# Optimization experiments

Measured on AMD Instinct MI355X. Metric: run time of the kernel, lower is better.

## Reference

```python
import jax, jax.numpy as jnp
import numpy as np

N_NODES = 30000
N_EDGES = 150000
N_REL = 10
IN_DIM = 256
OUT_DIM = 256


def setup_inputs() -> dict:
    key = jax.random.key(0)
    ks = jax.random.split(key, 10)
    s = 1.0 / np.sqrt(IN_DIM)  # ~nn.Linear init scale
    return {
        "x": jax.random.normal(ks[0], (N_NODES, IN_DIM), jnp.float32),
        "W_self": jax.random.uniform(ks[1], (IN_DIM, OUT_DIM), jnp.float32, -s, s),
        "b_self": jax.random.uniform(ks[2], (OUT_DIM,), jnp.float32, -s, s),
        "W_fwd": jax.random.uniform(ks[3], (N_REL, IN_DIM, OUT_DIM), jnp.float32, -s, s),
        "b_fwd": jax.random.uniform(ks[4], (N_REL, OUT_DIM), jnp.float32, -s, s),
        "W_rev": jax.random.uniform(ks[5], (N_REL, IN_DIM, OUT_DIM), jnp.float32, -s, s),
        "b_rev": jax.random.uniform(ks[6], (N_REL, OUT_DIM), jnp.float32, -s, s),
        "dep_idx": jax.random.randint(ks[7], (N_EDGES,), 0, N_NODES, jnp.int32),
        "rel_idx": jax.random.randint(ks[8], (N_EDGES,), 0, N_REL, jnp.int32),
        "gov_idx": jax.random.randint(ks[9], (N_EDGES,), 0, N_NODES, jnp.int32),
    }


def reference(x, W_self, b_self, W_fwd, b_fwd, W_rev, b_rev, dep_idx, rel_idx, gov_idx):
    # self transform for every token: [N, out]
    out = x @ W_self + b_self
    # transform all nodes by every relation weight up-front: [R, N, out]
    H_fwd = jnp.einsum("ni,rio->rno", x, W_fwd) + b_fwd[:, None, :]
    H_rev = jnp.einsum("ni,rio->rno", x, W_rev) + b_rev[:, None, :]
    # per-edge gather: forward msg uses governor feature, reverse msg uses dependent
    msg_fwd = H_fwd[rel_idx, gov_idx]  # [E, out]
    msg_rev = H_rev[rel_idx, dep_idx]  # [E, out]
    # scatter-add: forward msg -> dependent, reverse msg -> governor
    out = out.at[dep_idx].add(msg_fwd)
    out = out.at[gov_idx].add(msg_rev)
    return out
```

## Files before the change

kernel.cpp:

```cpp
#include <hip/hip_runtime.h>

#define N_NODES 30000
#define N_EDGES 150000
#define N_REL 10
#define DIM 256

#define SORT_BLOCKS 120
#define SORT_CHUNK ((N_EDGES + SORT_BLOCKS - 1) / SORT_BLOCKS)

#define SCAN_CHUNK 256
#define SCAN_BLOCKS ((N_NODES + SCAN_CHUNK - 1) / SCAN_CHUNK)

#define PREP_XB 7500
#define PREP_WB 5376
#define PREP_ZB 235

typedef __attribute__((ext_vector_type(8))) short bf16x8;
typedef __attribute__((ext_vector_type(4))) float f32x4;

__device__ __forceinline__ unsigned short f2bf(float f) {
  union { float f; unsigned int u; } v; v.f = f;
  unsigned int u = v.u;
  unsigned int r = u + 0x7fffu + ((u >> 16) & 1u);
  return (unsigned short)(r >> 16);
}


__global__ void prep_kernel(const float* __restrict__ x,
                            const float* __restrict__ Wf,
                            const float* __restrict__ Wr,
                            const float* __restrict__ Ws,
                            unsigned short* __restrict__ xbf,
                            unsigned short* __restrict__ wt,
                            int* __restrict__ cnt) {
  int b = blockIdx.x;
  if (b < PREP_XB) {
    int idx = b * 256 + threadIdx.x;
    float4 v = reinterpret_cast<const float4*>(x)[idx];
    ushort4 o;
    o.x = f2bf(v.x); o.y = f2bf(v.y); o.z = f2bf(v.z); o.w = f2bf(v.w);
    reinterpret_cast<ushort4*>(xbf)[idx] = o;
  } else if (b < PREP_XB + PREP_WB) {
    int idx = (b - PREP_XB) * 256 + threadIdx.x;
    int bb = idx >> 16;
    int t = idx & 65535;
    int o = t >> 8, i = t & 255;
    const float* src = (bb < N_REL) ? (Wf + (size_t)bb * 65536)
                     : (bb < 2 * N_REL) ? (Wr + (size_t)(bb - N_REL) * 65536)
                     : Ws;
    wt[idx] = f2bf(src[i * 256 + o]);
  } else {
    int i = (b - PREP_XB - PREP_WB) * 256 + threadIdx.x;
    if (i < 2 * N_NODES) cnt[i] = 0;
  }
}

__global__ void hist_all_kernel(const int* __restrict__ rel,
                                const int* __restrict__ dep,
                                const int* __restrict__ gov,
                                int* __restrict__ block_counts,
                                int* __restrict__ cnt) {
  __shared__ int h[N_REL];
  if (threadIdx.x < N_REL) h[threadIdx.x] = 0;
  __syncthreads();
  int beg = blockIdx.x * SORT_CHUNK;
  int end = min(beg + SORT_CHUNK, N_EDGES);
  for (int e = beg + threadIdx.x; e < end; e += blockDim.x) {
    atomicAdd(&h[rel[e]], 1);
    atomicAdd(&cnt[dep[e]], 1);
    atomicAdd(&cnt[N_NODES + gov[e]], 1);
  }
  __syncthreads();
  if (threadIdx.x < N_REL)
    block_counts[blockIdx.x * N_REL + threadIdx.x] = h[threadIdx.x];
}

__global__ void scan_rel_kernel(const int* __restrict__ block_counts,
                                int* __restrict__ rel_start,
                                int* __restrict__ block_offset) {
  __shared__ int tot[N_REL];
  int r = threadIdx.x;
  if (r < N_REL) {
    int s = 0;
    for (int b = 0; b < SORT_BLOCKS; ++b) s += block_counts[b * N_REL + r];
    tot[r] = s;
  }
  __syncthreads();
  if (threadIdx.x == 0) {
    int s = 0;
    for (int i = 0; i < N_REL; ++i) { rel_start[i] = s; s += tot[i]; }
    rel_start[N_REL] = s;
  }
  __syncthreads();
  if (r < N_REL) {
    int run = rel_start[r];
    for (int b = 0; b < SORT_BLOCKS; ++b) {
      block_offset[b * N_REL + r] = run;
      run += block_counts[b * N_REL + r];
    }
  }
}

__global__ void scanA_kernel(const int* __restrict__ cnt,
                             int* __restrict__ tmp, int* __restrict__ sums) {
  __shared__ int s[SCAN_CHUNK];
  int d = blockIdx.y, b = blockIdx.x, t = threadIdx.x;
  int i = b * SCAN_CHUNK + t;
  int v = (i < N_NODES) ? cnt[d * N_NODES + i] : 0;
  s[t] = v;
  __syncthreads();
  for (int off = 1; off < SCAN_CHUNK; off <<= 1) {
    int add = (t >= off) ? s[t - off] : 0;
    __syncthreads();
    s[t] += add;
    __syncthreads();
  }
  if (i < N_NODES) tmp[d * N_NODES + i] = s[t] - v;
  if (t == SCAN_CHUNK - 1) sums[d * SCAN_BLOCKS + b] = s[t];
}

__global__ void scanB_kernel(const int* __restrict__ sums,
                             int* __restrict__ chunk_off, int* __restrict__ rp) {
  __shared__ int s[128];
  int d = blockIdx.x, t = threadIdx.x;
  int v = (t < SCAN_BLOCKS) ? sums[d * SCAN_BLOCKS + t] : 0;
  s[t] = v;
  __syncthreads();
  for (int off = 1; off < 128; off <<= 1) {
    int add = (t >= off) ? s[t - off] : 0;
    __syncthreads();
    s[t] += add;
    __syncthreads();
  }
  if (t < SCAN_BLOCKS) chunk_off[d * SCAN_BLOCKS + t] = s[t] - v;
  if (t == 127) rp[d * (N_NODES + 1) + N_NODES] = s[127];
}

__global__ void scanC_kernel(const int* __restrict__ tmp,
                             const int* __restrict__ chunk_off,
                             int* __restrict__ rp, int* __restrict__ cursor) {
  int d = blockIdx.y;
  int i = blockIdx.x * SCAN_CHUNK + threadIdx.x;
  if (i < N_NODES) {
    int v = tmp[d * N_NODES + i] + chunk_off[d * SCAN_BLOCKS + blockIdx.x];
    rp[d * (N_NODES + 1) + i] = v;
    cursor[d * N_NODES + i] = v;
  }
}

__global__ void scatter_all_kernel(const int* __restrict__ rel,
                                   const int* __restrict__ dep,
                                   const int* __restrict__ gov,
                                   const int* __restrict__ block_offset,
                                   int* __restrict__ cursor,
                                   int* __restrict__ perm,
                                   int* __restrict__ srcf,
                                   int* __restrict__ srcr,
                                   int* __restrict__ colf,
                                   int* __restrict__ colr) {
  __shared__ int cur[N_REL];
  if (threadIdx.x < N_REL)
    cur[threadIdx.x] = block_offset[blockIdx.x * N_REL + threadIdx.x];
  __syncthreads();
  int beg = blockIdx.x * SORT_CHUNK;
  int end = min(beg + SORT_CHUNK, N_EDGES);
  for (int e = beg + threadIdx.x; e < end; e += blockDim.x) {
    int dp = dep[e], gv = gov[e];
    int pos = atomicAdd(&cur[rel[e]], 1);
    perm[pos] = e;
    srcf[pos] = gv;
    srcr[pos] = dp;
    colf[atomicAdd(&cursor[dp], 1)] = pos;
    colr[atomicAdd(&cursor[N_NODES + gv], 1)] = pos;
  }
}


__global__ __launch_bounds__(256, 2)
void mega_gemm_kernel(const unsigned short* __restrict__ xbf,
                      const unsigned short* __restrict__ wt,
                      const float* __restrict__ b_self,
                      const float* __restrict__ b_fwd,
                      const float* __restrict__ b_rev,
                      const int* __restrict__ srcf,
                      const int* __restrict__ srcr,
                      const int* __restrict__ rel_start,
                      unsigned short* __restrict__ msg,
                      float* __restrict__ out) {
  const int bkt = blockIdx.y;
  const bool is_self = (bkt >= 2 * N_REL);
  const bool fwd = bkt < N_REL;
  const int r = is_self ? 0 : (fwd ? bkt : bkt - N_REL);

  int beg, cnt;
  const int* src_arr = fwd ? srcf : srcr;
  unsigned short* mdir = msg + (fwd ? 0 : (size_t)N_EDGES * DIM);
  if (is_self) {
    beg = (bkt - 2 * N_REL) * (N_NODES / 2);
    cnt = N_NODES / 2;
  } else {
    beg = rel_start[r];
    cnt = rel_start[r + 1] - beg;
  }
  const int ntiles = (cnt + 63) >> 6;
  const int GX = gridDim.x;

  const int tid = threadIdx.x;
  const int wave = tid >> 6, lane = tid & 63;
  const int lm = lane & 15, q = lane >> 4;
  const int nb = wave * 64;
  const int half = lane >> 5;

  __shared__ int s_src[2][64];
  __shared__ unsigned short sA[2][64 * DIM];

  bf16x8 wf[8][4];
  const unsigned short* wbase =
      wt + (size_t)(is_self ? 2 * N_REL : bkt) * DIM * DIM;
  #pragma unroll
  for (int kk = 0; kk < 8; ++kk)
    #pragma unroll
    for (int ni = 0; ni < 4; ++ni)
      wf[kk][ni] = *reinterpret_cast<const bf16x8*>(
          wbase + (size_t)(nb + ni * 16 + lm) * DIM + kk * 32 + q * 8);

  const float* bptr = is_self ? b_self : ((fwd ? b_fwd : b_rev) + r * DIM);
  float bias[4];
  #pragma unroll
  for (int ni = 0; ni < 4; ++ni) bias[ni] = bptr[nb + ni * 16 + lm];

  int swz[8];
  #pragma unroll
  for (int i = 0; i < 8; ++i)
    swz[i] = (((lane & 31) ^ ((i * 2 + half) & 7)) * 8);
  int rowoff[4];
  #pragma unroll
  for (int mi = 0; mi < 4; ++mi) rowoff[mi] = (mi * 16 + lm) * DIM;
  int ckoff[8];
  #pragma unroll
  for (int kk = 0; kk < 8; ++kk)
    ckoff[kk] = ((kk * 4 + q) ^ (lm & 7)) * 8;

  int t = blockIdx.x;
  if (t >= ntiles) return;

  auto load_idx = [&](int tt) -> int {
    int tile0_ = tt << 6;
    if (is_self) {
      int rr = beg + tile0_ + tid;
      return rr < beg + cnt ? rr : beg + cnt - 1;
    } else {
      int p_ = tile0_ + tid;
      p_ = p_ < cnt ? p_ : cnt - 1;
      return src_arr[beg + p_];
    }
  };

  auto issue_stage = [&](int p) {
    const int* sp = s_src[p];
    unsigned short* db = sA[p];
    #pragma unroll
    for (int i = 0; i < 8; ++i) {
      int ldsrow = wave * 16 + i * 2;
      int rr = sp[ldsrow + half];
      const unsigned short* g = xbf + (size_t)rr * DIM + swz[i];
      __builtin_amdgcn_global_load_lds(
          (const __attribute__((address_space(1))) void*)g,
          (__attribute__((address_space(3))) void*)(db + ldsrow * DIM),
          16, 0, 0);
    }
  };

  auto step = [&](int cur) {
    const int tile0 = t << 6;
    const int rows_valid = min(64, cnt - tile0);
    const bool have_next = (t + GX) < ntiles;
    const bool have_next2 = (t + 2 * GX) < ntiles;

    __syncthreads();
    if (have_next) issue_stage(cur ^ 1);
    if (tid < 64 && have_next2) s_src[cur][tid] = load_idx(t + 2 * GX);

    f32x4 acc[4][4];
    #pragma unroll
    for (int mi = 0; mi < 4; ++mi)
      #pragma unroll
      for (int ni = 0; ni < 4; ++ni)
        acc[mi][ni] = (f32x4){0.f, 0.f, 0.f, 0.f};

    const unsigned short* sAb = sA[cur];
    #pragma unroll
    for (int kk = 0; kk < 8; ++kk) {
      bf16x8 a[4];
      #pragma unroll
      for (int mi = 0; mi < 4; ++mi)
        a[mi] = *reinterpret_cast<const bf16x8*>(sAb + rowoff[mi] + ckoff[kk]);
      #pragma unroll
      for (int mi = 0; mi < 4; ++mi)
        #pragma unroll
        for (int ni = 0; ni < 4; ++ni)
          acc[mi][ni] = __builtin_amdgcn_mfma_f32_16x16x32_bf16(
              a[mi], wf[kk][ni], acc[mi][ni], 0, 0, 0);
    }

    if (is_self) {
      #pragma unroll
      for (int mi = 0; mi < 4; ++mi) {
        #pragma unroll
        for (int reg = 0; reg < 4; ++reg) {
          int row = mi * 16 + q * 4 + reg;
          if (row < rows_valid) {
            #pragma unroll
            for (int ni = 0; ni < 4; ++ni)
              out[(size_t)(beg + tile0 + row) * DIM + nb + ni * 16 + lm] =
                  acc[mi][ni][reg] + bias[ni];
          }
        }
      }
    } else {
      #pragma unroll
      for (int mi = 0; mi < 4; ++mi) {
        #pragma unroll
        for (int reg = 0; reg < 4; ++reg) {
          int row = mi * 16 + q * 4 + reg;
          if (row < rows_valid) {
            unsigned int p0 = ((unsigned int)f2bf(acc[mi][1][reg] + bias[1]) << 16) |
                              f2bf(acc[mi][0][reg] + bias[0]);
            unsigned int p1 = ((unsigned int)f2bf(acc[mi][3][reg] + bias[3]) << 16) |
                              f2bf(acc[mi][2][reg] + bias[2]);
            uint2 u; u.x = p0; u.y = p1;
            *reinterpret_cast<uint2*>(
                mdir + (size_t)(beg + tile0 + row) * DIM + nb + lm * 4) = u;
          }
        }
      }
    }
  };

  if (tid < 64) s_src[0][tid] = load_idx(t);
  __syncthreads();
  issue_stage(0);
  if (tid < 64 && t + GX < ntiles) s_src[1][tid] = load_idx(t + GX);

  while (true) {
    step(0);
    t += GX; if (t >= ntiles) break;
    step(1);
    t += GX; if (t >= ntiles) break;
  }
}


__global__ void reduce_both_kernel(const unsigned short* __restrict__ msg,
                                   const int* __restrict__ rp,
                                   const int* __restrict__ colf,
                                   const int* __restrict__ colr,
                                   float* __restrict__ out) {
  const int n = blockIdx.x, t = threadIdx.x;
  const int g = t >> 6, lane = t & 63;
  const int b0 = rp[n], e0 = rp[n + 1];
  const int b1 = rp[(N_NODES + 1) + n], e1 = rp[(N_NODES + 1) + n + 1];
  if (e0 <= b0 && e1 <= b1) return;

  float a0 = 0.f, a1 = 0.f, a2 = 0.f, a3 = 0.f;
  for (int j = b0 + g; j < e0; j += 4) {
    int row = colf[j];
    uint2 v = *reinterpret_cast<const uint2*>(msg + (size_t)row * DIM + lane * 4);
    union { unsigned int u; float f; } c;
    c.u = v.x << 16;          a0 += c.f;
    c.u = v.x & 0xffff0000u;  a1 += c.f;
    c.u = v.y << 16;          a2 += c.f;
    c.u = v.y & 0xffff0000u;  a3 += c.f;
  }
  for (int j = b1 + g; j < e1; j += 4) {
    int row = colr[j];
    uint2 v = *reinterpret_cast<const uint2*>(
        msg + (size_t)(N_EDGES + row) * DIM + lane * 4);
    union { unsigned int u; float f; } c;
    c.u = v.x << 16;          a0 += c.f;
    c.u = v.x & 0xffff0000u;  a1 += c.f;
    c.u = v.y << 16;          a2 += c.f;
    c.u = v.y & 0xffff0000u;  a3 += c.f;
  }

  __shared__ float part[4][DIM];
  const int cb = (lane >> 4) * 64 + (lane & 15);
  part[g][cb +  0] = a0;
  part[g][cb + 16] = a1;
  part[g][cb + 32] = a2;
  part[g][cb + 48] = a3;
  __syncthreads();
  float s = part[0][t] + part[1][t] + part[2][t] + part[3][t];
  out[(size_t)n * DIM + t] += s;
}


__global__ __launch_bounds__(256, 2)
void self_gemm_kernel(const unsigned short* __restrict__ xbf,
                      const unsigned short* __restrict__ wt_self,
                      const float* __restrict__ b_self,
                      float* __restrict__ out) {
  const int tid = threadIdx.x;
  const int wave = tid >> 6, lane = tid & 63;
  const int lm = lane & 15, q = lane >> 4;
  const int nb = wave * 64;

  bf16x8 wf[8][4];
  #pragma unroll
  for (int kk = 0; kk < 8; ++kk)
    #pragma unroll
    for (int ni = 0; ni < 4; ++ni)
      wf[kk][ni] = *reinterpret_cast<const bf16x8*>(
          wt_self + (size_t)(nb + ni * 16 + lm) * DIM + kk * 32 + q * 8);

  float bias[4];
  #pragma unroll
  for (int ni = 0; ni < 4; ++ni) bias[ni] = b_self[nb + ni * 16 + lm];

  const int ntiles = (N_NODES + 63) / 64;
  for (int t = blockIdx.x; t < ntiles; t += gridDim.x) {
    const int row0 = t * 64;
    const unsigned short* xr[4];
    #pragma unroll
    for (int mi = 0; mi < 4; ++mi) {
      int r = row0 + mi * 16 + lm;
      int rc = r < N_NODES ? r : N_NODES - 1;
      xr[mi] = xbf + (size_t)rc * DIM + q * 8;
    }

    f32x4 acc[4][4];
    #pragma unroll
    for (int mi = 0; mi < 4; ++mi)
      #pragma unroll
      for (int ni = 0; ni < 4; ++ni)
        acc[mi][ni] = (f32x4){0.f, 0.f, 0.f, 0.f};

    #pragma unroll
    for (int kk = 0; kk < 8; ++kk) {
      bf16x8 a[4];
      #pragma unroll
      for (int mi = 0; mi < 4; ++mi)
        a[mi] = *reinterpret_cast<const bf16x8*>(xr[mi] + kk * 32);
      #pragma unroll
      for (int mi = 0; mi < 4; ++mi)
        #pragma unroll
        for (int ni = 0; ni < 4; ++ni)
          acc[mi][ni] = __builtin_amdgcn_mfma_f32_16x16x32_bf16(a[mi], wf[kk][ni], acc[mi][ni], 0, 0, 0);
    }

    #pragma unroll
    for (int mi = 0; mi < 4; ++mi) {
      #pragma unroll
      for (int reg = 0; reg < 4; ++reg) {
        int row = row0 + mi * 16 + q * 4 + reg;
        if (row < N_NODES) {
          #pragma unroll
          for (int ni = 0; ni < 4; ++ni)
            out[(size_t)row * DIM + nb + ni * 16 + lm] = acc[mi][ni][reg] + bias[ni];
        }
      }
    }
  }
}

__global__ void edge_gemm_atomic_kernel(const unsigned short* __restrict__ xbf,
                                        const unsigned short* __restrict__ wt,
                                        const float* __restrict__ b_fwd,
                                        const float* __restrict__ b_rev,
                                        const int* __restrict__ perm,
                                        const int* __restrict__ rel_start,
                                        const int* __restrict__ dep,
                                        const int* __restrict__ gov,
                                        float* __restrict__ out) {
  const int bucket = blockIdx.y;
  const int r = bucket % N_REL;
  const bool fwd = bucket < N_REL;
  const int beg = rel_start[r];
  const int cnt = rel_start[r + 1] - beg;
  const int ntiles = (cnt + 63) >> 6;

  const int tid = threadIdx.x;
  const int wave = tid >> 6, lane = tid & 63;
  const int lm = lane & 15, q = lane >> 4;
  const int nb = wave * 64;

  __shared__ int s_src[64], s_dst[64];

  const unsigned short* wr[4];
  #pragma unroll
  for (int ni = 0; ni < 4; ++ni)
    wr[ni] = wt + (size_t)bucket * DIM * DIM + (size_t)(nb + ni * 16 + lm) * DIM + q * 8;

  const float* bptr = (fwd ? b_fwd : b_rev) + r * DIM;
  float bias[4];
  #pragma unroll
  for (int ni = 0; ni < 4; ++ni) bias[ni] = bptr[nb + ni * 16 + lm];

  for (int t = blockIdx.x; t < ntiles; t += gridDim.x) {
    const int tile0 = t << 6;
    const int rows_valid = min(64, cnt - tile0);

    if (tid < 64) {
      int s = 0, d = -1;
      if (tid < rows_valid) {
        int e = perm[beg + tile0 + tid];
        int gv = gov[e], dp = dep[e];
        s = fwd ? gv : dp;
        d = fwd ? dp : gv;
      }
      s_src[tid] = s;
      s_dst[tid] = d;
    }
    __syncthreads();

    const unsigned short* xr[4];
    #pragma unroll
    for (int mi = 0; mi < 4; ++mi)
      xr[mi] = xbf + (size_t)s_src[mi * 16 + lm] * DIM + q * 8;

    f32x4 acc[4][4];
    #pragma unroll
    for (int mi = 0; mi < 4; ++mi)
      #pragma unroll
      for (int ni = 0; ni < 4; ++ni)
        acc[mi][ni] = (f32x4){0.f, 0.f, 0.f, 0.f};

    #pragma unroll
    for (int k0 = 0; k0 < DIM; k0 += 32) {
      bf16x8 a[4], b[4];
      #pragma unroll
      for (int mi = 0; mi < 4; ++mi) a[mi] = *reinterpret_cast<const bf16x8*>(xr[mi] + k0);
      #pragma unroll
      for (int ni = 0; ni < 4; ++ni) b[ni] = *reinterpret_cast<const bf16x8*>(wr[ni] + k0);
      #pragma unroll
      for (int mi = 0; mi < 4; ++mi)
        #pragma unroll
        for (int ni = 0; ni < 4; ++ni)
          acc[mi][ni] = __builtin_amdgcn_mfma_f32_16x16x32_bf16(a[mi], b[ni], acc[mi][ni], 0, 0, 0);
    }

    #pragma unroll
    for (int mi = 0; mi < 4; ++mi) {
      #pragma unroll
      for (int reg = 0; reg < 4; ++reg) {
        int row = mi * 16 + q * 4 + reg;
        if (row < rows_valid) {
          int dst = s_dst[row];
          float* op = out + (size_t)dst * DIM + nb + lm;
          #pragma unroll
          for (int ni = 0; ni < 4; ++ni)
            atomicAdd(op + ni * 16, acc[mi][ni][reg] + bias[ni]);
        }
      }
    }
    __syncthreads();
  }
}


extern "C" void kernel_launch(void* const* d_in, const int* in_sizes, int n_in,
                              void* d_out, int out_size, void* d_ws, size_t ws_size,
                              hipStream_t stream) {
  const float* x      = (const float*)d_in[0];
  const float* W_self = (const float*)d_in[1];
  const float* b_self = (const float*)d_in[2];
  const float* W_fwd  = (const float*)d_in[3];
  const float* b_fwd  = (const float*)d_in[4];
  const float* W_rev  = (const float*)d_in[5];
  const float* b_rev  = (const float*)d_in[6];
  const int* dep = (const int*)d_in[7];
  const int* rel = (const int*)d_in[8];
  const int* gov = (const int*)d_in[9];
  float* out = (float*)d_out;

  char* base = (char*)d_ws;
  size_t off = 0;
  auto alloc = [&](size_t bytes) -> char* {
    char* p = base + off;
    off = (off + bytes + 15) & ~(size_t)15;
    return p;
  };

  unsigned short* xbf = (unsigned short*)alloc((size_t)N_NODES * DIM * 2);
  unsigned short* wt  = (unsigned short*)alloc((size_t)21 * DIM * DIM * 2);
  int* perm          = (int*)alloc((size_t)N_EDGES * 4);
  int* srcf          = (int*)alloc((size_t)N_EDGES * 4);
  int* srcr          = (int*)alloc((size_t)N_EDGES * 4);
  int* rel_start     = (int*)alloc(16 * 4);
  int* block_counts  = (int*)alloc(SORT_BLOCKS * N_REL * 4);
  int* block_offset  = (int*)alloc(SORT_BLOCKS * N_REL * 4);
  int* cnt       = (int*)alloc((size_t)2 * N_NODES * 4);
  int* tmp       = (int*)alloc((size_t)2 * N_NODES * 4);
  int* sums      = (int*)alloc((size_t)2 * SCAN_BLOCKS * 4);
  int* chunk_off = (int*)alloc((size_t)2 * SCAN_BLOCKS * 4);
  int* rp        = (int*)alloc((size_t)2 * (N_NODES + 1) * 4);
  int* cursor    = (int*)alloc((size_t)2 * N_NODES * 4);
  int* colf      = (int*)alloc((size_t)N_EDGES * 4);
  int* colr      = (int*)alloc((size_t)N_EDGES * 4);
  unsigned short* msg = (unsigned short*)alloc((size_t)2 * N_EDGES * DIM * 2);
  const bool two_phase = (off <= ws_size);

  prep_kernel<<<PREP_XB + PREP_WB + PREP_ZB, 256, 0, stream>>>(
      x, W_fwd, W_rev, W_self, xbf, wt, cnt);
  hist_all_kernel<<<SORT_BLOCKS, 256, 0, stream>>>(rel, dep, gov, block_counts, cnt);
  scan_rel_kernel<<<1, 64, 0, stream>>>(block_counts, rel_start, block_offset);
  scanA_kernel<<<dim3(SCAN_BLOCKS, 2), SCAN_CHUNK, 0, stream>>>(cnt, tmp, sums);
  scanB_kernel<<<2, 128, 0, stream>>>(sums, chunk_off, rp);
  scanC_kernel<<<dim3(SCAN_BLOCKS, 2), SCAN_CHUNK, 0, stream>>>(tmp, chunk_off, rp, cursor);
  scatter_all_kernel<<<SORT_BLOCKS, 256, 0, stream>>>(
      rel, dep, gov, block_offset, cursor, perm, srcf, srcr, colf, colr);

  if (two_phase) {
    mega_gemm_kernel<<<dim3(48, 2 * N_REL + 2), 256, 0, stream>>>(
        xbf, wt, b_self, b_fwd, b_rev, srcf, srcr, rel_start, msg, out);
    reduce_both_kernel<<<N_NODES, 256, 0, stream>>>(msg, rp, colf, colr, out);
  } else {
    self_gemm_kernel<<<120, 256, 0, stream>>>(
        xbf, wt + (size_t)20 * DIM * DIM, b_self, out);
    edge_gemm_atomic_kernel<<<dim3(260, 20), 256, 0, stream>>>(
        xbf, wt, b_fwd, b_rev, perm, rel_start, dep, gov, out);
  }
}
```

Before: 288.3 us.

## Fuse preprocessing launches, restructure GEMM inner loop, one-wave-per-node reduce

Folds the edge histogram into the conversion kernel and the two small scan kernels plus the relation scan into one finish kernel, using a memset for the counters. This cuts the number of serial launches. The GEMM step now processes one 16-row group at a time with only 4 accumulators and brackets the MFMA run with s_setprio, meant to lower register pressure and favour matrix issue. The reduce kernel gives each node a single wave, unrolled by two edges, and drops the shared-memory cross-wave reduction. The trade-off is less memory-level parallelism for high-degree nodes and a serial per-block prefix loop in the scan.

New measurement: 265.8 us. 7.8% less time.

```diff
diff --git a/kernel.cpp b/kernel.cpp
--- a/kernel.cpp
+++ b/kernel.cpp
@@ -13,7 +13,6 @@
 
 #define PREP_XB 7500
 #define PREP_WB 5376
-#define PREP_ZB 235
 
 typedef __attribute__((ext_vector_type(8))) short bf16x8;
 typedef __attribute__((ext_vector_type(4))) float f32x4;
@@ -26,13 +25,17 @@
 }
 
 
-__global__ void prep_kernel(const float* __restrict__ x,
-                            const float* __restrict__ Wf,
-                            const float* __restrict__ Wr,
-                            const float* __restrict__ Ws,
-                            unsigned short* __restrict__ xbf,
-                            unsigned short* __restrict__ wt,
-                            int* __restrict__ cnt) {
+__global__ void prep_hist_kernel(const float* __restrict__ x,
+                                 const float* __restrict__ Wf,
+                                 const float* __restrict__ Wr,
+                                 const float* __restrict__ Ws,
+                                 const int* __restrict__ rel,
+                                 const int* __restrict__ dep,
+                                 const int* __restrict__ gov,
+                                 unsigned short* __restrict__ xbf,
+                                 unsigned short* __restrict__ wt,
+                                 int* __restrict__ block_counts,
+                                 int* __restrict__ cnt) {
   int b = blockIdx.x;
   if (b < PREP_XB) {
     int idx = b * 256 + threadIdx.x;
@@ -50,56 +53,23 @@
                      : Ws;
     wt[idx] = f2bf(src[i * 256 + o]);
   } else {
-    int i = (b - PREP_XB - PREP_WB) * 256 + threadIdx.x;
-    if (i < 2 * N_NODES) cnt[i] = 0;
-  }
-}
-
-__global__ void hist_all_kernel(const int* __restrict__ rel,
-                                const int* __restrict__ dep,
-                                const int* __restrict__ gov,
-                                int* __restrict__ block_counts,
-                                int* __restrict__ cnt) {
-  __shared__ int h[N_REL];
-  if (threadIdx.x < N_REL) h[threadIdx.x] = 0;
-  __syncthreads();
-  int beg = blockIdx.x * SORT_CHUNK;
-  int end = min(beg + SORT_CHUNK, N_EDGES);
-  for (int e = beg + threadIdx.x; e < end; e += blockDim.x) {
-    atomicAdd(&h[rel[e]], 1);
-    atomicAdd(&cnt[dep[e]], 1);
-    atomicAdd(&cnt[N_NODES + gov[e]], 1);
-  }
-  __syncthreads();
-  if (threadIdx.x < N_REL)
-    block_counts[blockIdx.x * N_REL + threadIdx.x] = h[threadIdx.x];
-}
-
-__global__ void scan_rel_kernel(const int* __restrict__ block_counts,
-                                int* __restrict__ rel_start,
-                                int* __restrict__ block_offset) {
-  __shared__ int tot[N_REL];
-  int r = threadIdx.x;
-  if (r < N_REL) {
-    int s = 0;
-    for (int b = 0; b < SORT_BLOCKS; ++b) s += block_counts[b * N_REL + r];
-    tot[r] = s;
-  }
-  __syncthreads();
-  if (threadIdx.x == 0) {
-    int s = 0;
-    for (int i = 0; i < N_REL; ++i) { rel_start[i] = s; s += tot[i]; }
-    rel_start[N_REL] = s;
-  }
-  __syncthreads();
-  if (r < N_REL) {
-    int run = rel_start[r];
-    for (int b = 0; b < SORT_BLOCKS; ++b) {
-      block_offset[b * N_REL + r] = run;
-      run += block_counts[b * N_REL + r];
-    }
-  }
-}
+    int hb = b - PREP_XB - PREP_WB;
+    __shared__ int h[N_REL];
+    if (threadIdx.x < N_REL) h[threadIdx.x] = 0;
+    __syncthreads();
+    int beg = hb * SORT_CHUNK;
+    int end = min(beg + SORT_CHUNK, N_EDGES);
+    for (int e = beg + threadIdx.x; e < end; e += blockDim.x) {
+      atomicAdd(&h[rel[e]], 1);
+      atomicAdd(&cnt[dep[e]], 1);
+      atomicAdd(&cnt[N_NODES + gov[e]], 1);
+    }
+    __syncthreads();
+    if (threadIdx.x < N_REL)
+      block_counts[hb * N_REL + threadIdx.x] = h[threadIdx.x];
+  }
+}
+
 
 __global__ void scanA_kernel(const int* __restrict__ cnt,
                              int* __restrict__ tmp, int* __restrict__ sums) {
@@ -119,34 +89,64 @@
   if (t == SCAN_CHUNK - 1) sums[d * SCAN_BLOCKS + b] = s[t];
 }
 
-__global__ void scanB_kernel(const int* __restrict__ sums,
-                             int* __restrict__ chunk_off, int* __restrict__ rp) {
-  __shared__ int s[128];
-  int d = blockIdx.x, t = threadIdx.x;
-  int v = (t < SCAN_BLOCKS) ? sums[d * SCAN_BLOCKS + t] : 0;
-  s[t] = v;
+
+__global__ void scan_finish_kernel(const int* __restrict__ sums,
+                                   const int* __restrict__ tmp,
+                                   const int* __restrict__ block_counts,
+                                   int* __restrict__ rp,
+                                   int* __restrict__ cursor,
+                                   int* __restrict__ rel_start,
+                                   int* __restrict__ block_offset) {
+  int d = blockIdx.y, b = blockIdx.x, t = threadIdx.x;
+
+  if (b == SCAN_BLOCKS) {
+    if (d == 1) return;
+    __shared__ int tot[N_REL];
+    __shared__ int rstart[N_REL + 1];
+    int r = t;
+    if (r < N_REL) {
+      int s = 0;
+      for (int bb = 0; bb < SORT_BLOCKS; ++bb) s += block_counts[bb * N_REL + r];
+      tot[r] = s;
+    }
+    __syncthreads();
+    if (t == 0) {
+      int s = 0;
+      for (int i = 0; i < N_REL; ++i) { rstart[i] = s; s += tot[i]; }
+      rstart[N_REL] = s;
+      for (int i = 0; i <= N_REL; ++i) rel_start[i] = rstart[i];
+    }
+    __syncthreads();
+    if (r < N_REL) {
+      int run = rstart[r];
+      for (int bb = 0; bb < SORT_BLOCKS; ++bb) {
+        block_offset[bb * N_REL + r] = run;
+        run += block_counts[bb * N_REL + r];
+      }
+    }
+    return;
+  }
+
+  __shared__ int ssum[SCAN_BLOCKS];
+  __shared__ int spre[SCAN_BLOCKS + 1];
+  if (t < SCAN_BLOCKS) ssum[t] = sums[d * SCAN_BLOCKS + t];
   __syncthreads();
-  for (int off = 1; off < 128; off <<= 1) {
-    int add = (t >= off) ? s[t - off] : 0;
-    __syncthreads();
-    s[t] += add;
-    __syncthreads();
-  }
-  if (t < SCAN_BLOCKS) chunk_off[d * SCAN_BLOCKS + t] = s[t] - v;
-  if (t == 127) rp[d * (N_NODES + 1) + N_NODES] = s[127];
-}
-
-__global__ void scanC_kernel(const int* __restrict__ tmp,
-                             const int* __restrict__ chunk_off,
-                             int* __restrict__ rp, int* __restrict__ cursor) {
-  int d = blockIdx.y;
-  int i = blockIdx.x * SCAN_CHUNK + threadIdx.x;
+  if (t == 0) {
+    int run = 0;
+    for (int i = 0; i < SCAN_BLOCKS; ++i) { spre[i] = run; run += ssum[i]; }
+    spre[SCAN_BLOCKS] = run;
+  }
+  __syncthreads();
+  int chunk = spre[b];
+  int i = b * SCAN_CHUNK + t;
   if (i < N_NODES) {
-    int v = tmp[d * N_NODES + i] + chunk_off[d * SCAN_BLOCKS + blockIdx.x];
+    int v = tmp[d * N_NODES + i] + chunk;
     rp[d * (N_NODES + 1) + i] = v;
     cursor[d * N_NODES + i] = v;
   }
-}
+  if (b == 0 && t == 0) rp[d * (N_NODES + 1) + N_NODES] = spre[SCAN_BLOCKS];
+}
+
 
 __global__ void scatter_all_kernel(const int* __restrict__ rel,
                                    const int* __restrict__ dep,
@@ -281,31 +281,28 @@
     if (have_next) issue_stage(cur ^ 1);
     if (tid < 64 && have_next2) s_src[cur][tid] = load_idx(t + 2 * GX);
 
-    f32x4 acc[4][4];
-    #pragma unroll
-    for (int mi = 0; mi < 4; ++mi)
-      #pragma unroll
-      for (int ni = 0; ni < 4; ++ni)
-        acc[mi][ni] = (f32x4){0.f, 0.f, 0.f, 0.f};
-
     const unsigned short* sAb = sA[cur];
     #pragma unroll
-    for (int kk = 0; kk < 8; ++kk) {
-      bf16x8 a[4];
-      #pragma unroll
-      for (int mi = 0; mi < 4; ++mi)
-        a[mi] = *reinterpret_cast<const bf16x8*>(sAb + rowoff[mi] + ckoff[kk]);
-      #pragma unroll
-      for (int mi = 0; mi < 4; ++mi)
+    for (int mi = 0; mi < 4; ++mi) {
+      bf16x8 a[8];
+      #pragma unroll
+      for (int kk = 0; kk < 8; ++kk)
+        a[kk] = *reinterpret_cast<const bf16x8*>(sAb + rowoff[mi] + ckoff[kk]);
+
+      f32x4 acc[4];
+      #pragma unroll
+      for (int ni = 0; ni < 4; ++ni) acc[ni] = (f32x4){0.f, 0.f, 0.f, 0.f};
+
+      __builtin_amdgcn_s_setprio(1);
+      #pragma unroll
+      for (int kk = 0; kk < 8; ++kk)
         #pragma unroll
         for (int ni = 0; ni < 4; ++ni)
-          acc[mi][ni] = __builtin_amdgcn_mfma_f32_16x16x32_bf16(
-              a[mi], wf[kk][ni], acc[mi][ni], 0, 0, 0);
-    }
-
-    if (is_self) {
-      #pragma unroll
-      for (int mi = 0; mi < 4; ++mi) {
+          acc[ni] = __builtin_amdgcn_mfma_f32_16x16x32_bf16(
+              a[kk], wf[kk][ni], acc[ni], 0, 0, 0);
+      __builtin_amdgcn_s_setprio(0);
+
+      if (is_self) {
         #pragma unroll
         for (int reg = 0; reg < 4; ++reg) {
           int row = mi * 16 + q * 4 + reg;
@@ -313,21 +310,18 @@
             #pragma unroll
             for (int ni = 0; ni < 4; ++ni)
               out[(size_t)(beg + tile0 + row) * DIM + nb + ni * 16 + lm] =
-                  acc[mi][ni][reg] + bias[ni];
+                  acc[ni][reg] + bias[ni];
           }
         }
-      }
-    } else {
-      #pragma unroll
-      for (int mi = 0; mi < 4; ++mi) {
+      } else {
         #pragma unroll
         for (int reg = 0; reg < 4; ++reg) {
           int row = mi * 16 + q * 4 + reg;
           if (row < rows_valid) {
-            unsigned int p0 = ((unsigned int)f2bf(acc[mi][1][reg] + bias[1]) << 16) |
-                              f2bf(acc[mi][0][reg] + bias[0]);
-            unsigned int p1 = ((unsigned int)f2bf(acc[mi][3][reg] + bias[3]) << 16) |
-                              f2bf(acc[mi][2][reg] + bias[2]);
+            unsigned int p0 = ((unsigned int)f2bf(acc[1][reg] + bias[1]) << 16) |
+                              f2bf(acc[0][reg] + bias[0]);
+            unsigned int p1 = ((unsigned int)f2bf(acc[3][reg] + bias[3]) << 16) |
+                              f2bf(acc[2][reg] + bias[2]);
             uint2 u; u.x = p0; u.y = p1;
             *reinterpret_cast<uint2*>(
                 mdir + (size_t)(beg + tile0 + row) * DIM + nb + lm * 4) = u;
@@ -356,42 +350,66 @@
                                    const int* __restrict__ colf,
                                    const int* __restrict__ colr,
                                    float* __restrict__ out) {
-  const int n = blockIdx.x, t = threadIdx.x;
-  const int g = t >> 6, lane = t & 63;
+  const int n = blockIdx.x * 4 + (threadIdx.x >> 6);
+  if (n >= N_NODES) return;
+  const int lane = threadIdx.x & 63;
   const int b0 = rp[n], e0 = rp[n + 1];
   const int b1 = rp[(N_NODES + 1) + n], e1 = rp[(N_NODES + 1) + n + 1];
-  if (e0 <= b0 && e1 <= b1) return;
+  if (e0 == b0 && e1 == b1) return;
 
   float a0 = 0.f, a1 = 0.f, a2 = 0.f, a3 = 0.f;
-  for (int j = b0 + g; j < e0; j += 4) {
-    int row = colf[j];
-    uint2 v = *reinterpret_cast<const uint2*>(msg + (size_t)row * DIM + lane * 4);
-    union { unsigned int u; float f; } c;
+  union { unsigned int u; float f; } c;
+
+  int j = b0;
+  for (; j + 1 < e0; j += 2) {
+    int r0 = colf[j], r1 = colf[j + 1];
+    uint2 v0 = *reinterpret_cast<const uint2*>(msg + (size_t)r0 * DIM + lane * 4);
+    uint2 v1 = *reinterpret_cast<const uint2*>(msg + (size_t)r1 * DIM + lane * 4);
+    c.u = v0.x << 16;          a0 += c.f;
+    c.u = v0.x & 0xffff0000u;  a1 += c.f;
+    c.u = v0.y << 16;          a2 += c.f;
+    c.u = v0.y & 0xffff0000u;  a3 += c.f;
+    c.u = v1.x << 16;          a0 += c.f;
+    c.u = v1.x & 0xffff0000u;  a1 += c.f;
+    c.u = v1.y << 16;          a2 += c.f;
+    c.u = v1.y & 0xffff0000u;  a3 += c.f;
+  }
+  if (j < e0) {
+    uint2 v = *reinterpret_cast<const uint2*>(msg + (size_t)colf[j] * DIM + lane * 4);
     c.u = v.x << 16;          a0 += c.f;
     c.u = v.x & 0xffff0000u;  a1 += c.f;
     c.u = v.y << 16;          a2 += c.f;
     c.u = v.y & 0xffff0000u;  a3 += c.f;
   }
-  for (int j = b1 + g; j < e1; j += 4) {
-    int row = colr[j];
-    uint2 v = *reinterpret_cast<const uint2*>(
-        msg + (size_t)(N_EDGES + row) * DIM + lane * 4);
-    union { unsigned int u; float f; } c;
+  const unsigned short* mrev = msg + (size_t)N_EDGES * DIM;
+  j = b1;
+  for (; j + 1 < e1; j += 2) {
+    int r0 = colr[j], r1 = colr[j + 1];
+    uint2 v0 = *reinterpret_cast<const uint2*>(mrev + (size_t)r0 * DIM + lane * 4);
+    uint2 v1 = *reinterpret_cast<const uint2*>(mrev + (size_t)r1 * DIM + lane * 4);
+    c.u = v0.x << 16;          a0 += c.f;
+    c.u = v0.x & 0xffff0000u;  a1 += c.f;
+    c.u = v0.y << 16;          a2 += c.f;
+    c.u = v0.y & 0xffff0000u;  a3 += c.f;
+    c.u = v1.x << 16;          a0 += c.f;
+    c.u = v1.x & 0xffff0000u;  a1 += c.f;
+    c.u = v1.y << 16;          a2 += c.f;
+    c.u = v1.y & 0xffff0000u;  a3 += c.f;
+  }
+  if (j < e1) {
+    uint2 v = *reinterpret_cast<const uint2*>(mrev + (size_t)colr[j] * DIM + lane * 4);
     c.u = v.x << 16;          a0 += c.f;
     c.u = v.x & 0xffff0000u;  a1 += c.f;
     c.u = v.y << 16;          a2 += c.f;
     c.u = v.y & 0xffff0000u;  a3 += c.f;
   }
 
-  __shared__ float part[4][DIM];
   const int cb = (lane >> 4) * 64 + (lane & 15);
-  part[g][cb +  0] = a0;
-  part[g][cb + 16] = a1;
-  part[g][cb + 32] = a2;
-  part[g][cb + 48] = a3;
-  __syncthreads();
-  float s = part[0][t] + part[1][t] + part[2][t] + part[3][t];
-  out[(size_t)n * DIM + t] += s;
+  float* op = out + (size_t)n * DIM;
+  op[cb +  0] += a0;
+  op[cb + 16] += a1;
+  op[cb + 32] += a2;
+  op[cb + 48] += a3;
 }
 
 
@@ -592,7 +610,6 @@
   int* cnt       = (int*)alloc((size_t)2 * N_NODES * 4);
   int* tmp       = (int*)alloc((size_t)2 * N_NODES * 4);
   int* sums      = (int*)alloc((size_t)2 * SCAN_BLOCKS * 4);
-  int* chunk_off = (int*)alloc((size_t)2 * SCAN_BLOCKS * 4);
   int* rp        = (int*)alloc((size_t)2 * (N_NODES + 1) * 4);
   int* cursor    = (int*)alloc((size_t)2 * N_NODES * 4);
   int* colf      = (int*)alloc((size_t)N_EDGES * 4);
@@ -600,20 +617,20 @@
   unsigned short* msg = (unsigned short*)alloc((size_t)2 * N_EDGES * DIM * 2);
   const bool two_phase = (off <= ws_size);
 
-  prep_kernel<<<PREP_XB + PREP_WB + PREP_ZB, 256, 0, stream>>>(
-      x, W_fwd, W_rev, W_self, xbf, wt, cnt);
-  hist_all_kernel<<<SORT_BLOCKS, 256, 0, stream>>>(rel, dep, gov, block_counts, cnt);
-  scan_rel_kernel<<<1, 64, 0, stream>>>(block_counts, rel_start, block_offset);
+  hipMemsetAsync(cnt, 0, (size_t)2 * N_NODES * 4, stream);
+  prep_hist_kernel<<<PREP_XB + PREP_WB + SORT_BLOCKS, 256, 0, stream>>>(
+      x, W_fwd, W_rev, W_self, rel, dep, gov, xbf, wt, block_counts, cnt);
   scanA_kernel<<<dim3(SCAN_BLOCKS, 2), SCAN_CHUNK, 0, stream>>>(cnt, tmp, sums);
-  scanB_kernel<<<2, 128, 0, stream>>>(sums, chunk_off, rp);
-  scanC_kernel<<<dim3(SCAN_BLOCKS, 2), SCAN_CHUNK, 0, stream>>>(tmp, chunk_off, rp, cursor);
+  scan_finish_kernel<<<dim3(SCAN_BLOCKS + 1, 2), SCAN_CHUNK, 0, stream>>>(
+      sums, tmp, block_counts, rp, cursor, rel_start, block_offset);
   scatter_all_kernel<<<SORT_BLOCKS, 256, 0, stream>>>(
       rel, dep, gov, block_offset, cursor, perm, srcf, srcr, colf, colr);
 
   if (two_phase) {
     mega_gemm_kernel<<<dim3(48, 2 * N_REL + 2), 256, 0, stream>>>(
         xbf, wt, b_self, b_fwd, b_rev, srcf, srcr, rel_start, msg, out);
-    reduce_both_kernel<<<N_NODES, 256, 0, stream>>>(msg, rp, colf, colr, out);
+    reduce_both_kernel<<<(N_NODES + 3) / 4, 256, 0, stream>>>(
+        msg, rp, colf, colr, out);
   } else {
     self_gemm_kernel<<<120, 256, 0, stream>>>(
         xbf, wt + (size_t)20 * DIM * DIM, b_self, out);
```
